# Kernel optimization log

Hardware: AMD Instinct MI355X
Metric: run time of the kernel (lower is better)

The kernel has to match this reference:

```python
import jax, jax.numpy as jnp
import numpy as np

N_HEADS = 16
HEAD_SIZE = 64
D_EMBD = 1024
BLOCK_SIZE = 1024
B, T = 4, 1024


def setup_inputs() -> dict:
    key = jax.random.key(0)
    ks = jax.random.split(key, 6)
    s = 0.02
    x = jax.random.normal(ks[0], (B, T, D_EMBD), dtype=jnp.float32)
    # per-head bias-free Q/K/V projections, stacked: [H, C, Hs]
    Wq = jax.random.normal(ks[1], (N_HEADS, D_EMBD, HEAD_SIZE), dtype=jnp.float32) * s
    Wk = jax.random.normal(ks[2], (N_HEADS, D_EMBD, HEAD_SIZE), dtype=jnp.float32) * s
    Wv = jax.random.normal(ks[3], (N_HEADS, D_EMBD, HEAD_SIZE), dtype=jnp.float32) * s
    # output projection W_o: Linear(d_embd, d_embd) with bias
    Wo = jax.random.normal(ks[4], (D_EMBD, D_EMBD), dtype=jnp.float32) * s
    bo = jax.random.normal(ks[5], (D_EMBD,), dtype=jnp.float32) * s
    return {"x": x, "Wq": Wq, "Wk": Wk, "Wv": Wv, "Wo": Wo, "bo": bo}


def reference(x, Wq, Wk, Wv, Wo, bo):
    # Batched equivalent of the per-head loop: q,k,v: [B, H, T, Hs]
    q = jnp.einsum('btc,hcs->bhts', x, Wq)
    k = jnp.einsum('btc,hcs->bhts', x, Wk)
    v = jnp.einsum('btc,hcs->bhts', x, Wv)
    scale = 1.0 / jnp.sqrt(jnp.asarray(HEAD_SIZE, dtype=x.dtype))
    scores = jnp.einsum('bhts,bhus->bhtu', q, k) * scale  # [B,H,T,T]
    causal = jnp.tril(jnp.ones((T, T), dtype=bool))
    scores = jnp.where(causal[None, None, :, :], scores, jnp.asarray(-jnp.inf, dtype=x.dtype))
    wei = jax.nn.softmax(scores, axis=-1)  # dropout p=0.0 -> identity
    out = jnp.einsum('bhtu,bhus->bhts', wei, v)  # [B,H,T,Hs]
    out = out.transpose(0, 2, 1, 3).reshape(B, T, D_EMBD)  # concat heads
    return out @ Wo.T + bo  # final Linear; dropout p=0.0 -> identity
```

## Files before the change

kernel.cpp:

```cpp
#include <hip/hip_runtime.h>
#include <hip/hip_bf16.h>
#include <math.h>

#define NH 16
#define HS 64
#define DE 1024
#define TT 1024
#define BBATCH 4
#define MTOK 4096

typedef __bf16 v8bf __attribute__((ext_vector_type(8)));
typedef __bf16 v4bf __attribute__((ext_vector_type(4)));
typedef float  v4f  __attribute__((ext_vector_type(4)));

__device__ __forceinline__ void gl_lds16(const __bf16* g, __bf16* l) {
    __builtin_amdgcn_global_load_lds(
        (const __attribute__((address_space(1))) unsigned int*)g,
        (__attribute__((address_space(3))) unsigned int*)l, 16, 0, 0);
}

__global__ __launch_bounds__(256) void cast_bf16_kernel(
    const float* __restrict__ in, __bf16* __restrict__ out, int n4)
{
    int i = blockIdx.x * 256 + threadIdx.x;
    if (i >= n4) return;
    float4 v = ((const float4*)in)[i];
    v4bf o;
    o[0] = (__bf16)v.x; o[1] = (__bf16)v.y; o[2] = (__bf16)v.z; o[3] = (__bf16)v.w;
    *(v4bf*)&out[(size_t)i * 4] = o;
}

__global__ __launch_bounds__(256) void prep_w_kernel(
    const float* __restrict__ Wq, const float* __restrict__ Wk,
    const float* __restrict__ Wv, __bf16* __restrict__ Wt)
{
    int m = blockIdx.z, h = blockIdx.y, c0 = blockIdx.x * 64;
    const float* W = (m == 0) ? Wq : (m == 1) ? Wk : Wv;
    __shared__ float tile[64][65];
    int t = threadIdx.x;
    #pragma unroll
    for (int pp = 0; pp < 16; ++pp) {
        int cl = pp * 4 + (t >> 6);
        int s  = t & 63;
        tile[cl][s] = W[((size_t)h * DE + c0 + cl) * HS + s];
    }
    __syncthreads();
    #pragma unroll
    for (int pp = 0; pp < 16; ++pp) {
        int s  = pp * 4 + (t >> 6);
        int cl = t & 63;
        Wt[((size_t)(m * DE + h * HS + s)) * DE + c0 + cl] = (__bf16)tile[cl][s];
    }
}

__global__ __launch_bounds__(256) void gemm_bt_kernel(
    const __bf16* __restrict__ A, const __bf16* __restrict__ Bt,
    int K, int mode,
    __bf16* __restrict__ qk_out, __bf16* __restrict__ vt_out,
    float* __restrict__ f_out, const float* __restrict__ bias)
{
    __shared__ __align__(16) __bf16 As[128 * 64];
    __shared__ __align__(16) __bf16 Bs[128 * 64];
    const int tid = threadIdx.x;
    const int w = tid >> 6, l = tid & 63;
    const int wm = w >> 1, wn = w & 1;
    const int lhi = l >> 4, llo = l & 15;
    const int bm = blockIdx.y, bn = blockIdx.x;

    v4f acc[4][4];
    #pragma unroll
    for (int i = 0; i < 4; ++i)
        #pragma unroll
        for (int j = 0; j < 4; ++j)
            #pragma unroll
            for (int r = 0; r < 4; ++r) acc[i][j][r] = 0.f;

    const __bf16* Ab = A  + (size_t)bm * 128 * K;
    const __bf16* Bb = Bt + (size_t)bn * 128 * K;

    for (int k0 = 0; k0 < K; k0 += 64) {
        __syncthreads();
        #pragma unroll
        for (int i = 0; i < 4; ++i) {
            int chunk = i * 256 + w * 64 + l;
            gl_lds16(Ab + (size_t)(chunk >> 3) * K + k0 + (chunk & 7) * 8,
                     &As[(i * 256 + w * 64) * 8]);
            gl_lds16(Bb + (size_t)(chunk >> 3) * K + k0 + (chunk & 7) * 8,
                     &Bs[(i * 256 + w * 64) * 8]);
        }
        __syncthreads();
        #pragma unroll
        for (int kk = 0; kk < 64; kk += 32) {
            v8bf a[4], b[4];
            #pragma unroll
            for (int i = 0; i < 4; ++i)
                a[i] = *(const v8bf*)&As[(wm * 64 + i * 16 + llo) * 64 + kk + lhi * 8];
            #pragma unroll
            for (int j = 0; j < 4; ++j)
                b[j] = *(const v8bf*)&Bs[(wn * 64 + j * 16 + llo) * 64 + kk + lhi * 8];
            #pragma unroll
            for (int i = 0; i < 4; ++i)
                #pragma unroll
                for (int j = 0; j < 4; ++j)
                    acc[i][j] = __builtin_amdgcn_mfma_f32_16x16x32_bf16(a[i], b[j], acc[i][j], 0, 0, 0);
        }
    }

    const int row0 = bm * 128 + wm * 64;
    const int col0 = bn * 128 + wn * 64;

    if (mode == 0) {
        if (col0 < 2048) {
            #pragma unroll
            for (int i = 0; i < 4; ++i) {
                int rbase = row0 + i * 16 + lhi * 4;
                #pragma unroll
                for (int j = 0; j < 4; ++j) {
                    int c = col0 + j * 16 + llo;
                    #pragma unroll
                    for (int r = 0; r < 4; ++r)
                        qk_out[(size_t)(rbase + r) * 2048 + c] = (__bf16)acc[i][j][r];
                }
            }
        } else {
            #pragma unroll
            for (int i = 0; i < 4; ++i) {
                int rbase = row0 + i * 16 + lhi * 4;
                int bidx = rbase >> 10, t0 = rbase & 1023;
                #pragma unroll
                for (int j = 0; j < 4; ++j) {
                    int c = col0 + j * 16 + llo - 2048;
                    v4bf pk;
                    #pragma unroll
                    for (int r = 0; r < 4; ++r) pk[r] = (__bf16)acc[i][j][r];
                    *(v4bf*)&vt_out[((size_t)(bidx * NH + (c >> 6)) * HS + (c & 63)) * TT + t0] = pk;
                }
            }
        }
    } else {
        #pragma unroll
        for (int j = 0; j < 4; ++j) {
            int c = col0 + j * 16 + llo;
            float bv = bias[c];
            #pragma unroll
            for (int i = 0; i < 4; ++i) {
                int rbase = row0 + i * 16 + lhi * 4;
                #pragma unroll
                for (int r = 0; r < 4; ++r)
                    f_out[(size_t)(rbase + r) * DE + c] = acc[i][j][r] + bv;
            }
        }
    }
}

__device__ __forceinline__ v4f bf_mfma(v8bf a, v8bf b, v4f c) {
    return __builtin_amdgcn_mfma_f32_16x16x32_bf16(a, b, c, 0, 0, 0);
}

__device__ __forceinline__ void stage_kv(
    const __bf16* __restrict__ kb, const __bf16* __restrict__ vb,
    __bf16* Ksb, __bf16* Vsb, int k0, int tid)
{
    #pragma unroll
    for (int i = 0; i < 2; ++i) {
        int c = i * 256 + tid;
        gl_lds16(kb + (size_t)(k0 + (c >> 3)) * 2048 + (c & 7) * 8, Ksb + c * 8);
        gl_lds16(vb + (size_t)(c >> 3) * TT + k0 + (c & 7) * 8,     Vsb + c * 8);
    }
}

template<bool DIAG>
__device__ __forceinline__ void attn_compute(
    const __bf16* __restrict__ Ksb, const __bf16* __restrict__ Vsb,
    __bf16* __restrict__ PsW, int k0, int r0, int lhi, int llo,
    v8bf aq0, v8bf aq1, v4f (&o)[4], float (&l_part)[4])
{
    v4f sacc[4];
    #pragma unroll
    for (int n = 0; n < 4; ++n)
        #pragma unroll
        for (int r = 0; r < 4; ++r) sacc[n][r] = 0.f;
    #pragma unroll
    for (int n = 0; n < 4; ++n) {
        v8bf bk0 = *(const v8bf*)&Ksb[(n * 16 + llo) * 64 + lhi * 8];
        v8bf bk1 = *(const v8bf*)&Ksb[(n * 16 + llo) * 64 + 32 + lhi * 8];
        sacc[n] = bf_mfma(aq0, bk0, sacc[n]);
        sacc[n] = bf_mfma(aq1, bk1, sacc[n]);
    }

    float prob[4][4];
    #pragma unroll
    for (int n = 0; n < 4; ++n) {
        int colg = k0 + n * 16 + llo;
        #pragma unroll
        for (int r = 0; r < 4; ++r) {
            float s2 = sacc[n][r] * 0.18033688f;
            if (DIAG) { int rowg = r0 + lhi * 4 + r; if (colg > rowg) s2 = -1e30f; }
            float p = exp2f(s2);
            prob[n][r] = p;
            l_part[r] += p;
        }
    }

    #pragma unroll
    for (int r = 0; r < 4; ++r)
        #pragma unroll
        for (int n = 0; n < 4; ++n)
            PsW[(lhi * 4 + r) * 72 + n * 16 + llo] = (__bf16)prob[n][r];

    #pragma unroll
    for (int kk = 0; kk < 64; kk += 32) {
        v8bf ap = *(const v8bf*)&PsW[llo * 72 + kk + lhi * 8];
        #pragma unroll
        for (int n = 0; n < 4; ++n) {
            v8bf bv = *(const v8bf*)&Vsb[(n * 16 + llo) * 64 + kk + lhi * 8];
            o[n] = bf_mfma(ap, bv, o[n]);
        }
    }
}

__global__ __launch_bounds__(256) void attn_kernel(
    const __bf16* __restrict__ qk, const __bf16* __restrict__ vt,
    __bf16* __restrict__ att)
{
    __shared__ __align__(16) __bf16 Ks[2][64 * 64];
    __shared__ __align__(16) __bf16 Vs[2][64 * 64];
    __shared__ __align__(16) __bf16 Ps[4][16 * 72];

    const int tid = threadIdx.x;
    const int w = tid >> 6, l = tid & 63;
    const int lhi = l >> 4, llo = l & 15;
    const int bh = blockIdx.x & 63;
    const int qt = 15 - (blockIdx.x >> 6);
    const int b = bh >> 4, h = bh & 15;

    const __bf16* qbase = qk + (size_t)b * TT * 2048 + h * HS;
    const __bf16* kbase = qk + (size_t)b * TT * 2048 + 1024 + h * HS;
    const __bf16* vbase = vt + (size_t)bh * HS * TT;
    __bf16* PsW = &Ps[w][0];

    const int r0 = qt * 64 + w * 16;

    stage_kv(kbase, vbase, Ks[0], Vs[0], 0, tid);

    v8bf aq0 = *(const v8bf*)&qbase[(size_t)(r0 + llo) * 2048 + lhi * 8];
    v8bf aq1 = *(const v8bf*)&qbase[(size_t)(r0 + llo) * 2048 + 32 + lhi * 8];

    float l_part[4] = {0.f, 0.f, 0.f, 0.f};
    v4f o[4];
    #pragma unroll
    for (int n = 0; n < 4; ++n)
        #pragma unroll
        for (int r = 0; r < 4; ++r) o[n][r] = 0.f;

    for (int kt = 0; kt < qt; ++kt) {
        const int buf = kt & 1;
        __syncthreads();
        stage_kv(kbase, vbase, Ks[buf ^ 1], Vs[buf ^ 1], (kt + 1) * 64, tid);
        attn_compute<false>(Ks[buf], Vs[buf], PsW, kt * 64, r0, lhi, llo, aq0, aq1, o, l_part);
    }
    __syncthreads();
    attn_compute<true>(Ks[qt & 1], Vs[qt & 1], PsW, qt * 64, r0, lhi, llo, aq0, aq1, o, l_part);

    #pragma unroll
    for (int r = 0; r < 4; ++r) {
        float s = l_part[r];
        #pragma unroll
        for (int msk = 1; msk < 16; msk <<= 1) s += __shfl_xor(s, msk, 64);
        float inv = 1.f / s;
        int rowg = b * TT + r0 + lhi * 4 + r;
        #pragma unroll
        for (int n = 0; n < 4; ++n)
            att[(size_t)rowg * DE + h * HS + n * 16 + llo] = (__bf16)(o[n][r] * inv);
    }
}

extern "C" void kernel_launch(void* const* d_in, const int* in_sizes, int n_in,
                              void* d_out, int out_size, void* d_ws, size_t ws_size,
                              hipStream_t stream)
{
    const float* x  = (const float*)d_in[0];
    const float* Wq = (const float*)d_in[1];
    const float* Wk = (const float*)d_in[2];
    const float* Wv = (const float*)d_in[3];
    const float* Wo = (const float*)d_in[4];
    const float* bo = (const float*)d_in[5];
    float* out = (float*)d_out;

    char* ws = (char*)d_ws;
    __bf16* xb  = (__bf16*)(ws);
    __bf16* Wt  = (__bf16*)(ws + 8388608);
    __bf16* Wob = (__bf16*)(ws + 14680064);
    __bf16* qk  = (__bf16*)(ws + 16777216);
    __bf16* vt  = (__bf16*)(ws + 33554432);
    __bf16* att = (__bf16*)(ws + 41943040);

    cast_bf16_kernel<<<4096, 256, 0, stream>>>(x, xb, 1048576);
    prep_w_kernel<<<dim3(16, 16, 3), 256, 0, stream>>>(Wq, Wk, Wv, Wt);
    cast_bf16_kernel<<<1024, 256, 0, stream>>>(Wo, Wob, 262144);
    gemm_bt_kernel<<<dim3(24, 32), 256, 0, stream>>>(xb, Wt, 1024, 0, qk, vt, nullptr, nullptr);
    attn_kernel<<<1024, 256, 0, stream>>>(qk, vt, att);
    gemm_bt_kernel<<<dim3(8, 32), 256, 0, stream>>>(att, Wob, 1024, 1, nullptr, nullptr, out, bo);
}
```

Before: 193.8 us.

## Double-buffer GEMM LDS tiles and remap blocks for XCD locality

The projection GEMM kernel now uses two LDS buffers per operand. The next K-tile is issued via global_load_lds while the current tile feeds the MFMAs, which halves the barriers per iteration and hides global-load latency. The 2D grid becomes a 1D launch whose block index is remapped so blocks landing on the same XCD share A row-tiles, to improve L2 reuse. The cost is double the LDS footprint per block, which may lower occupancy, and correctness relies on the barrier waiting for the asynchronous LDS loads.

```diff
diff --git a/kernel.cpp b/kernel.cpp
--- a/kernel.cpp
+++ b/kernel.cpp
@@ -53,56 +53,71 @@
     }
 }
 
+__device__ __forceinline__ void gemm_stage(
+    const __bf16* __restrict__ Ab, const __bf16* __restrict__ Bb,
+    __bf16* As, __bf16* Bs, int K, int k0, int w, int l)
+{
+    #pragma unroll
+    for (int i = 0; i < 4; ++i) {
+        int chunk = i * 256 + w * 64 + l;
+        gl_lds16(Ab + (size_t)(chunk >> 3) * K + k0 + (chunk & 7) * 8,
+                 As + (i * 256 + w * 64) * 8);
+        gl_lds16(Bb + (size_t)(chunk >> 3) * K + k0 + (chunk & 7) * 8,
+                 Bs + (i * 256 + w * 64) * 8);
+    }
+}
+
 __global__ __launch_bounds__(256) void gemm_bt_kernel(
     const __bf16* __restrict__ A, const __bf16* __restrict__ Bt,
     int K, int mode,
     __bf16* __restrict__ qk_out, __bf16* __restrict__ vt_out,
     float* __restrict__ f_out, const float* __restrict__ bias)
 {
-    __shared__ __align__(16) __bf16 As[128 * 64];
-    __shared__ __align__(16) __bf16 Bs[128 * 64];
+    __shared__ __align__(16) __bf16 As[2][128 * 64];
+    __shared__ __align__(16) __bf16 Bs[2][128 * 64];
     const int tid = threadIdx.x;
     const int w = tid >> 6, l = tid & 63;
     const int wm = w >> 1, wn = w & 1;
     const int lhi = l >> 4, llo = l & 15;
-    const int bm = blockIdx.y, bn = blockIdx.x;
+
+    const int lin = blockIdx.x;
+    const int xcd = lin & 7, j = lin >> 3;
+    const int bm = xcd * 4 + (j & 3);
+    const int bn = j >> 2;
 
     v4f acc[4][4];
     #pragma unroll
     for (int i = 0; i < 4; ++i)
         #pragma unroll
-        for (int j = 0; j < 4; ++j)
-            #pragma unroll
-            for (int r = 0; r < 4; ++r) acc[i][j][r] = 0.f;
+        for (int jj = 0; jj < 4; ++jj)
+            #pragma unroll
+            for (int r = 0; r < 4; ++r) acc[i][jj][r] = 0.f;
 
     const __bf16* Ab = A  + (size_t)bm * 128 * K;
     const __bf16* Bb = Bt + (size_t)bn * 128 * K;
 
-    for (int k0 = 0; k0 < K; k0 += 64) {
+    const int niter = K >> 6;
+    gemm_stage(Ab, Bb, As[0], Bs[0], K, 0, w, l);
+
+    for (int it = 0; it < niter; ++it) {
+        const int buf = it & 1;
         __syncthreads();
-        #pragma unroll
-        for (int i = 0; i < 4; ++i) {
-            int chunk = i * 256 + w * 64 + l;
-            gl_lds16(Ab + (size_t)(chunk >> 3) * K + k0 + (chunk & 7) * 8,
-                     &As[(i * 256 + w * 64) * 8]);
-            gl_lds16(Bb + (size_t)(chunk >> 3) * K + k0 + (chunk & 7) * 8,
-                     &Bs[(i * 256 + w * 64) * 8]);
-        }
-        __syncthreads();
+        if (it + 1 < niter)
+            gemm_stage(Ab, Bb, As[buf ^ 1], Bs[buf ^ 1], K, (it + 1) * 64, w, l);
         #pragma unroll
         for (int kk = 0; kk < 64; kk += 32) {
             v8bf a[4], b[4];
             #pragma unroll
             for (int i = 0; i < 4; ++i)
-                a[i] = *(const v8bf*)&As[(wm * 64 + i * 16 + llo) * 64 + kk + lhi * 8];
-            #pragma unroll
-            for (int j = 0; j < 4; ++j)
-                b[j] = *(const v8bf*)&Bs[(wn * 64 + j * 16 + llo) * 64 + kk + lhi * 8];
+                a[i] = *(const v8bf*)&As[buf][(wm * 64 + i * 16 + llo) * 64 + kk + lhi * 8];
+            #pragma unroll
+            for (int jj = 0; jj < 4; ++jj)
+                b[jj] = *(const v8bf*)&Bs[buf][(wn * 64 + jj * 16 + llo) * 64 + kk + lhi * 8];
             #pragma unroll
             for (int i = 0; i < 4; ++i)
                 #pragma unroll
-                for (int j = 0; j < 4; ++j)
-                    acc[i][j] = __builtin_amdgcn_mfma_f32_16x16x32_bf16(a[i], b[j], acc[i][j], 0, 0, 0);
+                for (int jj = 0; jj < 4; ++jj)
+                    acc[i][jj] = __builtin_amdgcn_mfma_f32_16x16x32_bf16(a[i], b[jj], acc[i][jj], 0, 0, 0);
         }
     }
 
@@ -115,11 +130,11 @@
             for (int i = 0; i < 4; ++i) {
                 int rbase = row0 + i * 16 + lhi * 4;
                 #pragma unroll
-                for (int j = 0; j < 4; ++j) {
-                    int c = col0 + j * 16 + llo;
+                for (int jj = 0; jj < 4; ++jj) {
+                    int c = col0 + jj * 16 + llo;
                     #pragma unroll
                     for (int r = 0; r < 4; ++r)
-                        qk_out[(size_t)(rbase + r) * 2048 + c] = (__bf16)acc[i][j][r];
+                        qk_out[(size_t)(rbase + r) * 2048 + c] = (__bf16)acc[i][jj][r];
                 }
             }
         } else {
@@ -128,26 +143,26 @@
                 int rbase = row0 + i * 16 + lhi * 4;
                 int bidx = rbase >> 10, t0 = rbase & 1023;
                 #pragma unroll
-                for (int j = 0; j < 4; ++j) {
-                    int c = col0 + j * 16 + llo - 2048;
+                for (int jj = 0; jj < 4; ++jj) {
+                    int c = col0 + jj * 16 + llo - 2048;
                     v4bf pk;
                     #pragma unroll
-                    for (int r = 0; r < 4; ++r) pk[r] = (__bf16)acc[i][j][r];
+                    for (int r = 0; r < 4; ++r) pk[r] = (__bf16)acc[i][jj][r];
                     *(v4bf*)&vt_out[((size_t)(bidx * NH + (c >> 6)) * HS + (c & 63)) * TT + t0] = pk;
                 }
             }
         }
     } else {
         #pragma unroll
-        for (int j = 0; j < 4; ++j) {
-            int c = col0 + j * 16 + llo;
+        for (int jj = 0; jj < 4; ++jj) {
+            int c = col0 + jj * 16 + llo;
             float bv = bias[c];
             #pragma unroll
             for (int i = 0; i < 4; ++i) {
                 int rbase = row0 + i * 16 + lhi * 4;
                 #pragma unroll
                 for (int r = 0; r < 4; ++r)
-                    f_out[(size_t)(rbase + r) * DE + c] = acc[i][j][r] + bv;
+                    f_out[(size_t)(rbase + r) * DE + c] = acc[i][jj][r] + bv;
             }
         }
     }
@@ -298,7 +313,7 @@
     cast_bf16_kernel<<<4096, 256, 0, stream>>>(x, xb, 1048576);
     prep_w_kernel<<<dim3(16, 16, 3), 256, 0, stream>>>(Wq, Wk, Wv, Wt);
     cast_bf16_kernel<<<1024, 256, 0, stream>>>(Wo, Wob, 262144);
-    gemm_bt_kernel<<<dim3(24, 32), 256, 0, stream>>>(xb, Wt, 1024, 0, qk, vt, nullptr, nullptr);
+    gemm_bt_kernel<<<768, 256, 0, stream>>>(xb, Wt, 1024, 0, qk, vt, nullptr, nullptr);
     attn_kernel<<<1024, 256, 0, stream>>>(qk, vt, att);
-    gemm_bt_kernel<<<dim3(8, 32), 256, 0, stream>>>(att, Wob, 1024, 1, nullptr, nullptr, out, bo);
-}
+    gemm_bt_kernel<<<256, 256, 0, stream>>>(att, Wob, 1024, 1, nullptr, nullptr, out, bo);
+}
```

New measurement: 187.0 us. 3.5% less time.
